# Kernel optimization log

Hardware: AMD Instinct MI355X
Metric: run time of the kernel (lower is better)

The kernel has to match this reference:

```python
import jax, jax.numpy as jnp
import numpy as np

NUM_HEADS = 8


def setup_inputs() -> dict:
    key = jax.random.key(0)
    k1, k2, k3 = jax.random.split(key, 3)
    B, D, H, W = 2, 256, 64, 64
    x = jax.random.normal(k1, (B, D, H, W), dtype=jnp.float32)
    w_qkv = jax.random.normal(k2, (3 * D, D), dtype=jnp.float32) * (D ** -0.5)
    b_qkv = jnp.zeros((3 * D,), dtype=jnp.float32)
    w_proj = jax.random.normal(k3, (D, D), dtype=jnp.float32) * (D ** -0.5)
    b_proj = jnp.zeros((D,), dtype=jnp.float32)
    return {"x": x, "w_qkv": w_qkv, "b_qkv": b_qkv, "w_proj": w_proj, "b_proj": b_proj}


def reference(x, w_qkv, b_qkv, w_proj, b_proj):
    B, D, H, W = x.shape
    N = H * W
    nh = NUM_HEADS
    hd = D // nh
    scale = hd ** -0.5
    # 1x1 conv == per-pixel linear: (B, 3D, H, W)
    qkv = jnp.einsum('od,bdhw->bohw', w_qkv, x) + b_qkv[None, :, None, None]
    # reshape (B, 3, nh, hd, N) then permute to (3, B, nh, N, hd)
    qkv = qkv.reshape(B, 3, nh, hd, N).transpose(1, 0, 2, 4, 3)
    q, k, v = qkv[0], qkv[1], qkv[2]          # each (B, nh, N, hd)
    attn = jnp.einsum('bhnd,bhmd->bhnm', q, k) * scale  # (B, nh, N, N)
    attn = jax.nn.softmax(attn, axis=-1)
    out = jnp.einsum('bhnm,bhmd->bhnd', attn, v)        # (B, nh, N, hd)
    out = out.transpose(0, 1, 3, 2).reshape(B, D, H, W)  # (B, nh, hd, N) -> (B, D, H, W)
    out = jnp.einsum('od,bdhw->bohw', w_proj, out) + b_proj[None, :, None, None]
    return out
```

## Files before the change

kernel.cpp:

```cpp
#include <hip/hip_runtime.h>

typedef unsigned short u16;
typedef unsigned int u32;
typedef float f32x4 __attribute__((ext_vector_type(4)));
typedef float f32x16 __attribute__((ext_vector_type(16)));
typedef __bf16 bf16x8 __attribute__((ext_vector_type(8)));
typedef int i32x4 __attribute__((ext_vector_type(4)));

#define DEV static __device__ __forceinline__

DEV u16 f2bf(float f){
  u32 u = __builtin_bit_cast(u32, f);
  u = (u + 0x7fffu + ((u >> 16) & 1u)) >> 16;
  return (u16)u;
}

DEV float fexp2(float x){
#if __has_builtin(__builtin_amdgcn_exp2f)
  return __builtin_amdgcn_exp2f(x);
#else
  return __builtin_exp2f(x);
#endif
}

DEV void async16(const void* g, void* l){
  __builtin_amdgcn_global_load_lds((const __attribute__((address_space(1))) void*)g,
                                   (__attribute__((address_space(3))) void*)l, 16, 0, 0);
}

static constexpr int NB = 2, DM = 256, NS = 4096, NH = 8, HD = 32;
static constexpr float QSCALE = 0.17677669529663687f * 1.4426950408889634f;
static constexpr float CAP = 24.0f;

__global__ __launch_bounds__(256) void k_transpose_x(const float* __restrict__ x, u16* __restrict__ xT){
  __shared__ float tile[64][65];
  int b = blockIdx.z, dt = blockIdx.y, nt = blockIdx.x;
  int t = threadIdx.x, tr = t >> 4, tc = t & 15;
  const float* src = x + ((size_t)b*DM + dt*64)*NS + nt*64;
#pragma unroll
  for(int rr=0; rr<4; ++rr){
    int row = rr*16 + tr;
    float4 v = *(const float4*)(src + (size_t)row*NS + tc*4);
    tile[row][tc*4+0]=v.x; tile[row][tc*4+1]=v.y; tile[row][tc*4+2]=v.z; tile[row][tc*4+3]=v.w;
  }
  __syncthreads();
#pragma unroll
  for(int rr=0; rr<4; ++rr){
    int nl = rr*16 + tr, dl = tc*4;
    ushort4 o;
    o.x = f2bf(tile[dl+0][nl]); o.y = f2bf(tile[dl+1][nl]);
    o.z = f2bf(tile[dl+2][nl]); o.w = f2bf(tile[dl+3][nl]);
    *(ushort4*)(xT + ((size_t)b*NS + nt*64 + nl)*DM + dt*64 + dl) = o;
  }
}

__global__ __launch_bounds__(256) void k_convert(const float* __restrict__ s, u16* __restrict__ d, int n4){
  int i = blockIdx.x*256 + threadIdx.x;
  if(i < n4){
    float4 v = ((const float4*)s)[i];
    ushort4 o; o.x=f2bf(v.x); o.y=f2bf(v.y); o.z=f2bf(v.z); o.w=f2bf(v.w);
    ((ushort4*)d)[i] = o;
  }
}

template<int MODE>
__global__ __launch_bounds__(256) void k_gemm(const u16* __restrict__ A, const u16* __restrict__ W,
                       const float* __restrict__ bias,
                       u16* __restrict__ q, u16* __restrict__ kbuf, u16* __restrict__ vt,
                       float* __restrict__ outp){
  __shared__ __align__(16) u16 ldsA[32768];
  __shared__ __align__(16) u16 ldsW[32768];
  int b = blockIdx.z, nt = blockIdx.x, ot = blockIdx.y;
  int tid = threadIdx.x;
  const char* Ab = (const char*)(A + ((size_t)b*NS + nt*128)*DM);
  const char* Wb = (const char*)(W + (size_t)ot*128*DM);
#pragma unroll
  for(int it=0; it<16; ++it){
    int dst = it*4096 + tid*16;
    int srcb = dst ^ (((dst >> 9) & 15) << 4);
    async16(Ab + srcb, (char*)ldsA + dst);
    async16(Wb + srcb, (char*)ldsW + dst);
  }
  __syncthreads();
  int w = tid >> 6, l = tid & 63, l15 = l & 15, g = l >> 4;
  f32x4 acc[2][8];
#pragma unroll
  for(int m=0;m<2;++m)
#pragma unroll
    for(int j=0;j<8;++j) acc[m][j] = f32x4{0.f,0.f,0.f,0.f};
#pragma unroll
  for(int kk=0; kk<8; ++kk){
    int cb = kk*64 + g*16;
    bf16x8 a[2], bb[8];
#pragma unroll
    for(int m=0;m<2;++m){
      int row = w*32 + m*16 + l15;
      a[m] = *(const bf16x8*)((const char*)ldsA + row*512 + (cb ^ ((row & 15) << 4)));
    }
#pragma unroll
    for(int j=0;j<8;++j){
      int row = j*16 + l15;
      bb[j] = *(const bf16x8*)((const char*)ldsW + row*512 + (cb ^ ((row & 15) << 4)));
    }
#pragma unroll
    for(int m=0;m<2;++m)
#pragma unroll
      for(int j=0;j<8;++j)
        acc[m][j] = __builtin_amdgcn_mfma_f32_16x16x32_bf16(a[m], bb[j], acc[m][j], 0, 0, 0);
  }

  if constexpr (MODE == 0){
    if(ot < 4){
      float sc = (ot < 2) ? QSCALE : 1.f;
      u16* dst = (ot < 2) ? q : kbuf;
      int hbase = (ot & 1) * 4;
      __syncthreads();
      char* tile = (char*)ldsA;
#pragma unroll
      for(int m=0;m<2;++m){
#pragma unroll
        for(int j=0;j<8;++j){
          int o = j*16 + l15;
          float bs = bias[ot*128 + o];
          float v0 = (acc[m][j][0]+bs)*sc, v1 = (acc[m][j][1]+bs)*sc;
          float v2 = (acc[m][j][2]+bs)*sc, v3 = (acc[m][j][3]+bs)*sc;
          u32 pA, pB;
          asm("v_cvt_pk_bf16_f32 %0, %1, %2" : "=v"(pA) : "v"(v0), "v"(v1));
          asm("v_cvt_pk_bf16_f32 %0, %1, %2" : "=v"(pB) : "v"(v2), "v"(v3));
          int n0 = w*32 + m*16 + g*4;
          *(u16*)(tile + (n0+0)*256 + ((o*2) ^ (((n0+0)&7)<<4))) = (u16)pA;
          *(u16*)(tile + (n0+1)*256 + ((o*2) ^ (((n0+1)&7)<<4))) = (u16)(pA>>16);
          *(u16*)(tile + (n0+2)*256 + ((o*2) ^ (((n0+2)&7)<<4))) = (u16)pB;
          *(u16*)(tile + (n0+3)*256 + ((o*2) ^ (((n0+3)&7)<<4))) = (u16)(pB>>16);
        }
      }
      __syncthreads();
#pragma unroll
      for(int p=0;p<2;++p){
        int seg = p*256 + tid;
        int hsub = seg >> 7, n_l = seg & 127;
        u16* gdst = dst + (((size_t)b*NH + hbase + hsub)*NS + nt*128 + n_l)*HD;
#pragma unroll
        for(int c=0;c<4;++c)
          *(uint4*)((char*)gdst + c*16) =
            *(const uint4*)(tile + n_l*256 + ((hsub*64 + c*16) ^ ((n_l&7)<<4)));
      }
    } else {
#pragma unroll
      for(int m=0;m<2;++m){
        int n0 = nt*128 + w*32 + m*16 + g*4;
#pragma unroll
        for(int j=0;j<8;++j){
          int o = ot*128 + j*16 + l15;
          float bs = bias[o];
          int hh = (o >> 5) & 7, dh = o & 31;
          float v0=acc[m][j][0]+bs, v1=acc[m][j][1]+bs, v2=acc[m][j][2]+bs, v3=acc[m][j][3]+bs;
          u32 pA, pB;
          asm("v_cvt_pk_bf16_f32 %0, %1, %2" : "=v"(pA) : "v"(v0), "v"(v1));
          asm("v_cvt_pk_bf16_f32 %0, %1, %2" : "=v"(pB) : "v"(v2), "v"(v3));
          uint2 pk; pk.x = pA; pk.y = pB;
          *(uint2*)(vt + (((size_t)b*NH + hh)*HD + dh)*NS + n0) = pk;
        }
      }
    }
  } else {
    __syncthreads();
    char* tileF = (char*)ldsA;
#pragma unroll
    for(int m=0;m<2;++m){
#pragma unroll
      for(int j=0;j<8;++j){
        int o = j*16 + l15;
        float bs = bias[ot*128 + o];
        f32x4 v4;
        v4[0]=acc[m][j][0]+bs; v4[1]=acc[m][j][1]+bs;
        v4[2]=acc[m][j][2]+bs; v4[3]=acc[m][j][3]+bs;
        int n0 = w*32 + m*16 + g*4;
        *(f32x4*)(tileF + o*512 + ((n0*4) ^ ((o&7)<<4))) = v4;
      }
    }
    __syncthreads();
#pragma unroll
    for(int p=0;p<4;++p){
      int idx = p*256 + tid;
      int o = idx >> 3, c = idx & 7;
      float* gdst = outp + ((size_t)b*DM + ot*128 + o)*NS + nt*128 + c*16;
#pragma unroll
      for(int u=0;u<4;++u)
        *(uint4*)((char*)gdst + u*16) =
          *(const uint4*)(tileF + o*512 + ((c*64 + u*16) ^ ((o&7)<<4)));
    }
  }
}

__global__ __launch_bounds__(256) void k_attn(const u16* __restrict__ Q, const u16* __restrict__ K,
                       const u16* __restrict__ V, u16* __restrict__ aout){
  __shared__ __align__(16) char lds[32768];
  char* ldsK = lds;
  char* ldsV = lds + 16384;
  int qt = blockIdx.x, bh = blockIdx.y;
  int tid = threadIdx.x, w = tid >> 6, l = tid & 63, l31 = l & 31, hi = l >> 5;
  int kh = w >> 1, qsub = w & 1;
  const u16* Qb = Q + (size_t)bh*NS*HD;
  const u16* Kb = K + (size_t)bh*NS*HD;
  const u16* Vb = V + (size_t)bh*HD*NS;
  int q0w = qt*64 + qsub*32;

  bf16x8 qf[2];
#pragma unroll
  for(int c=0;c<2;++c)
    qf[c] = *(const bf16x8*)(Qb + (size_t)(q0w + l31)*HD + c*16 + hi*8);

  int si = tid >> 7, idx = tid & 127;
  int krow = idx >> 1, khalf = idx & 1;
  int vd = idx >> 2, vch = idx & 3;
  const u16* kg = Kb + (size_t)(si*2048 + krow)*HD + khalf*16;
  const u16* vg = Vb + (size_t)vd*NS + si*2048 + vch*16;
  int kswz0 = (khalf*32 +  0) ^ (((krow >> 1) & 3) << 4);
  int kswz1 = (khalf*32 + 16) ^ (((krow >> 1) & 3) << 4);
  int vswz0 = (vch*32 +  0) ^ ((vd & 7) << 4);
  int vswz1 = (vch*32 + 16) ^ ((vd & 7) << 4);
  char* klw0 = ldsK + si*4096 + krow*64;
  char* vlw0 = ldsV + si*4096 + vd*128;

  {
    uint4 k0 = *(const uint4*)(kg);
    uint4 k1 = *(const uint4*)(kg + 8);
    uint4 v0 = *(const uint4*)(vg);
    uint4 v1 = *(const uint4*)(vg + 8);
    *(uint4*)(klw0 + kswz0) = k0;
    *(uint4*)(klw0 + kswz1) = k1;
    *(uint4*)(vlw0 + vswz0) = v0;
    *(uint4*)(vlw0 + vswz1) = v1;
  }
  __syncthreads();

  f32x16 OT;
#pragma unroll
  for(int r=0;r<16;++r) OT[r] = 0.f;
  f32x16 capv;
#pragma unroll
  for(int r=0;r<16;++r) capv[r] = -CAP;
  float psum = 0.f;

  const char* kfb = ldsK + kh*4096 + l31*64;
  const char* vfb = ldsV + kh*4096 + l31*128;
  int kswA = (hi*16) ^ (((l31 >> 1) & 3) << 4);
  int kswB = (32 + hi*16) ^ (((l31 >> 1) & 3) << 4);

  for(int t=0; t<32; ++t){
    int buf = t & 1;
    uint4 k0, k1, v0, v1;
    if(t < 31){
      const u16* kgt = kg + (size_t)(t+1)*64*HD;
      const u16* vgt = vg + (t+1)*64;
      k0 = *(const uint4*)(kgt); k1 = *(const uint4*)(kgt + 8);
      v0 = *(const uint4*)(vgt); v1 = *(const uint4*)(vgt + 8);
    }
    const char* kf = kfb + buf*8192;
    const char* vf = vfb + buf*8192;
#pragma unroll
    for(int sub=0; sub<2; ++sub){
      bf16x8 ka0 = *(const bf16x8*)(kf + sub*2048 + kswA);
      bf16x8 ka1 = *(const bf16x8*)(kf + sub*2048 + kswB);
      f32x16 st = __builtin_amdgcn_mfma_f32_32x32x16_bf16(ka0, qf[0], capv, 0, 0, 0);
      st = __builtin_amdgcn_mfma_f32_32x32x16_bf16(ka1, qf[1], st, 0, 0, 0);
#pragma unroll
      for(int r=0;r<16;++r) st[r] = fexp2(st[r]);
      {
        float a0 = (st[0]+st[1]) + (st[2]+st[3]);
        float a1 = (st[4]+st[5]) + (st[6]+st[7]);
        float a2 = (st[8]+st[9]) + (st[10]+st[11]);
        float a3 = (st[12]+st[13]) + (st[14]+st[15]);
        psum += (a0+a1) + (a2+a3);
      }
#pragma unroll
      for(int kk=0; kk<2; ++kk){
        int rb = kk*8;
        u32 XA, XB, YA, YB;
        asm("v_cvt_pk_bf16_f32 %0, %1, %2" : "=v"(XA) : "v"(st[rb+0]), "v"(st[rb+1]));
        asm("v_cvt_pk_bf16_f32 %0, %1, %2" : "=v"(XB) : "v"(st[rb+2]), "v"(st[rb+3]));
        asm("v_cvt_pk_bf16_f32 %0, %1, %2" : "=v"(YA) : "v"(st[rb+4]), "v"(st[rb+5]));
        asm("v_cvt_pk_bf16_f32 %0, %1, %2" : "=v"(YB) : "v"(st[rb+6]), "v"(st[rb+7]));
        asm("v_permlane32_swap_b32 %0, %1" : "+v"(XA), "+v"(YA));
        asm("v_permlane32_swap_b32 %0, %1" : "+v"(XB), "+v"(YB));
        i32x4 pw; pw[0] = (int)XA; pw[1] = (int)XB; pw[2] = (int)YA; pw[3] = (int)YB;
        bf16x8 pfrag = __builtin_bit_cast(bf16x8, pw);
        bf16x8 va = *(const bf16x8*)(vf + ((sub*64 + kk*32 + hi*16) ^ ((l31 & 7) << 4)));
        OT = __builtin_amdgcn_mfma_f32_32x32x16_bf16(va, pfrag, OT, 0, 0, 0);
      }
    }
    if(t < 31){
      char* klw = klw0 + (buf^1)*8192;
      char* vlw = vlw0 + (buf^1)*8192;
      *(uint4*)(klw + kswz0) = k0;
      *(uint4*)(klw + kswz1) = k1;
      *(uint4*)(vlw + vswz0) = v0;
      *(uint4*)(vlw + vswz1) = v1;
    }
    __syncthreads();
  }

  float* scrF = (float*)ldsK;
  float* scrS = (float*)ldsV;
  u16* obuf = (u16*)(ldsV + 256);
  float psum2 = psum + __shfl_xor(psum, 32, 64);
  if(kh == 1){
#pragma unroll
    for(int r=0;r<16;++r){
      int dd = (r & 3) + 8*(r >> 2) + 4*hi;
      scrF[qsub*1024 + dd*32 + l31] = OT[r];
    }
    if(hi == 0) scrS[qsub*32 + l31] = psum2;
  }
  __syncthreads();
  if(kh == 0){
    float total = psum2 + scrS[qsub*32 + l31];
    float inv = 1.0f / total;
#pragma unroll
    for(int r=0;r<16;r+=2){
      int dd = (r & 3) + 8*(r >> 2) + 4*hi;
      float o0 = (OT[r]   + scrF[qsub*1024 + dd*32 + l31]) * inv;
      float o1 = (OT[r+1] + scrF[qsub*1024 + (dd+1)*32 + l31]) * inv;
      u32 pk;
      asm("v_cvt_pk_bf16_f32 %0, %1, %2" : "=v"(pk) : "v"(o0), "v"(o1));
      *(u32*)((char*)obuf + (qsub*32 + l31)*64 + dd*2) = pk;
    }
  }
  __syncthreads();
  {
    int b = bh >> 3, h = bh & 7;
    int qq = tid >> 2, ch = tid & 3;
    uint4 vv = *(const uint4*)((const char*)obuf + qq*64 + ch*16);
    *(uint4*)((char*)aout + (((size_t)b*NS + qt*64 + qq)*DM + h*HD)*2 + ch*16) = vv;
  }
}

extern "C" void kernel_launch(void* const* d_in, const int* in_sizes, int n_in,
                              void* d_out, int out_size, void* d_ws, size_t ws_size,
                              hipStream_t stream) {
  (void)in_sizes; (void)n_in; (void)out_size; (void)ws_size;
  const float* x     = (const float*)d_in[0];
  const float* wqkv  = (const float*)d_in[1];
  const float* bqkv  = (const float*)d_in[2];
  const float* wproj = (const float*)d_in[3];
  const float* bproj = (const float*)d_in[4];
  float* out = (float*)d_out;
  char* ws = (char*)d_ws;
  u16* xT  = (u16*)(ws);
  u16* wqb = (u16*)(ws + 4194304);
  u16* wpb = (u16*)(ws + 4587520);
  u16* Q   = (u16*)(ws + 4718592);
  u16* K   = (u16*)(ws + 8912896);
  u16* Vt  = (u16*)(ws + 13107200);
  u16* aout = xT;

  k_transpose_x<<<dim3(64,4,2), 256, 0, stream>>>(x, xT);
  k_convert<<<192, 256, 0, stream>>>(wqkv, wqb, 49152);
  k_convert<<<64, 256, 0, stream>>>(wproj, wpb, 16384);
  k_gemm<0><<<dim3(32,6,2), 256, 0, stream>>>(xT, wqb, bqkv, Q, K, Vt, nullptr);
  k_attn<<<dim3(64,16), 256, 0, stream>>>(Q, K, Vt, aout);
  k_gemm<1><<<dim3(32,2,2), 256, 0, stream>>>(aout, wpb, bproj, nullptr, nullptr, nullptr, out);
}
```

Before: 157.0 us.

## Read K/V directly from global in attention, split keys over 4 waves, fuse prep kernels

The attention kernel no longer stages K and V tiles in LDS with double buffering and barriers. Each wave now loads its MFMA operands straight from global memory, relying on L2 and cache reuse. The block grows to 512 threads, with the key range split four ways, and partial outputs and sums are reduced through LDS. Separately, the x transpose and the two weight conversions are merged into one launch to cut launch overhead. The cost is uncoalesced per-lane global loads and no explicit prefetch overlap, though the barriers go away.

```diff
diff --git a/kernel.cpp b/kernel.cpp
--- a/kernel.cpp
+++ b/kernel.cpp
@@ -32,31 +32,35 @@
 static constexpr float QSCALE = 0.17677669529663687f * 1.4426950408889634f;
 static constexpr float CAP = 24.0f;
 
-__global__ __launch_bounds__(256) void k_transpose_x(const float* __restrict__ x, u16* __restrict__ xT){
+__global__ __launch_bounds__(256) void k_prep(const float* __restrict__ x, u16* __restrict__ xT,
+                      const float* __restrict__ wqkv, u16* __restrict__ wqb,
+                      const float* __restrict__ wproj, u16* __restrict__ wpb){
   __shared__ float tile[64][65];
-  int b = blockIdx.z, dt = blockIdx.y, nt = blockIdx.x;
-  int t = threadIdx.x, tr = t >> 4, tc = t & 15;
-  const float* src = x + ((size_t)b*DM + dt*64)*NS + nt*64;
-#pragma unroll
-  for(int rr=0; rr<4; ++rr){
-    int row = rr*16 + tr;
-    float4 v = *(const float4*)(src + (size_t)row*NS + tc*4);
-    tile[row][tc*4+0]=v.x; tile[row][tc*4+1]=v.y; tile[row][tc*4+2]=v.z; tile[row][tc*4+3]=v.w;
-  }
-  __syncthreads();
-#pragma unroll
-  for(int rr=0; rr<4; ++rr){
-    int nl = rr*16 + tr, dl = tc*4;
-    ushort4 o;
-    o.x = f2bf(tile[dl+0][nl]); o.y = f2bf(tile[dl+1][nl]);
-    o.z = f2bf(tile[dl+2][nl]); o.w = f2bf(tile[dl+3][nl]);
-    *(ushort4*)(xT + ((size_t)b*NS + nt*64 + nl)*DM + dt*64 + dl) = o;
-  }
-}
-
-__global__ __launch_bounds__(256) void k_convert(const float* __restrict__ s, u16* __restrict__ d, int n4){
-  int i = blockIdx.x*256 + threadIdx.x;
-  if(i < n4){
+  int bid = blockIdx.x, t = threadIdx.x;
+  if(bid < 512){
+    int b = bid >> 8, dt = (bid >> 6) & 3, nt = bid & 63;
+    int tr = t >> 4, tc = t & 15;
+    const float* src = x + ((size_t)b*DM + dt*64)*NS + nt*64;
+#pragma unroll
+    for(int rr=0; rr<4; ++rr){
+      int row = rr*16 + tr;
+      float4 v = *(const float4*)(src + (size_t)row*NS + tc*4);
+      tile[row][tc*4+0]=v.x; tile[row][tc*4+1]=v.y; tile[row][tc*4+2]=v.z; tile[row][tc*4+3]=v.w;
+    }
+    __syncthreads();
+#pragma unroll
+    for(int rr=0; rr<4; ++rr){
+      int nl = rr*16 + tr, dl = tc*4;
+      ushort4 o;
+      o.x = f2bf(tile[dl+0][nl]); o.y = f2bf(tile[dl+1][nl]);
+      o.z = f2bf(tile[dl+2][nl]); o.w = f2bf(tile[dl+3][nl]);
+      *(ushort4*)(xT + ((size_t)b*NS + nt*64 + nl)*DM + dt*64 + dl) = o;
+    }
+  } else {
+    int cid = bid - 512;
+    const float* s; u16* d; int i;
+    if(cid < 192){ s = wqkv; d = wqb; i = cid*256 + t; }
+    else         { s = wproj; d = wpb; i = (cid-192)*256 + t; }
     float4 v = ((const float4*)s)[i];
     ushort4 o; o.x=f2bf(v.x); o.y=f2bf(v.y); o.z=f2bf(v.z); o.w=f2bf(v.w);
     ((ushort4*)d)[i] = o;
@@ -193,47 +197,25 @@
   }
 }
 
-__global__ __launch_bounds__(256) void k_attn(const u16* __restrict__ Q, const u16* __restrict__ K,
+__global__ __launch_bounds__(512, 6) void k_attn(const u16* __restrict__ Q, const u16* __restrict__ K,
                        const u16* __restrict__ V, u16* __restrict__ aout){
-  __shared__ __align__(16) char lds[32768];
-  char* ldsK = lds;
-  char* ldsV = lds + 16384;
+  __shared__ float scrO[2][4][32][32];
+  __shared__ float scrS[2][4][32];
+  __shared__ __align__(8) u16 obuf[64][36];
   int qt = blockIdx.x, bh = blockIdx.y;
-  int tid = threadIdx.x, w = tid >> 6, l = tid & 63, l31 = l & 31, hi = l >> 5;
-  int kh = w >> 1, qsub = w & 1;
+  int tid = threadIdx.x, wid = tid >> 6, l = tid & 63, l31 = l & 31, hi = l >> 5;
+  int qsub = wid & 1, kq = wid >> 1;
   const u16* Qb = Q + (size_t)bh*NS*HD;
   const u16* Kb = K + (size_t)bh*NS*HD;
   const u16* Vb = V + (size_t)bh*HD*NS;
-  int q0w = qt*64 + qsub*32;
+  int q0 = qt*64 + qsub*32;
 
   bf16x8 qf[2];
-#pragma unroll
-  for(int c=0;c<2;++c)
-    qf[c] = *(const bf16x8*)(Qb + (size_t)(q0w + l31)*HD + c*16 + hi*8);
-
-  int si = tid >> 7, idx = tid & 127;
-  int krow = idx >> 1, khalf = idx & 1;
-  int vd = idx >> 2, vch = idx & 3;
-  const u16* kg = Kb + (size_t)(si*2048 + krow)*HD + khalf*16;
-  const u16* vg = Vb + (size_t)vd*NS + si*2048 + vch*16;
-  int kswz0 = (khalf*32 +  0) ^ (((krow >> 1) & 3) << 4);
-  int kswz1 = (khalf*32 + 16) ^ (((krow >> 1) & 3) << 4);
-  int vswz0 = (vch*32 +  0) ^ ((vd & 7) << 4);
-  int vswz1 = (vch*32 + 16) ^ ((vd & 7) << 4);
-  char* klw0 = ldsK + si*4096 + krow*64;
-  char* vlw0 = ldsV + si*4096 + vd*128;
-
-  {
-    uint4 k0 = *(const uint4*)(kg);
-    uint4 k1 = *(const uint4*)(kg + 8);
-    uint4 v0 = *(const uint4*)(vg);
-    uint4 v1 = *(const uint4*)(vg + 8);
-    *(uint4*)(klw0 + kswz0) = k0;
-    *(uint4*)(klw0 + kswz1) = k1;
-    *(uint4*)(vlw0 + vswz0) = v0;
-    *(uint4*)(vlw0 + vswz1) = v1;
-  }
-  __syncthreads();
+  qf[0] = *(const bf16x8*)(Qb + (size_t)(q0 + l31)*HD + hi*8);
+  qf[1] = *(const bf16x8*)(Qb + (size_t)(q0 + l31)*HD + 16 + hi*8);
+
+  const u16* kp = Kb + (size_t)(kq*1024 + l31)*HD + hi*8;
+  const u16* vp = Vb + (size_t)l31*NS + kq*1024 + hi*8;
 
   f32x16 OT;
 #pragma unroll
@@ -243,26 +225,12 @@
   for(int r=0;r<16;++r) capv[r] = -CAP;
   float psum = 0.f;
 
-  const char* kfb = ldsK + kh*4096 + l31*64;
-  const char* vfb = ldsV + kh*4096 + l31*128;
-  int kswA = (hi*16) ^ (((l31 >> 1) & 3) << 4);
-  int kswB = (32 + hi*16) ^ (((l31 >> 1) & 3) << 4);
-
-  for(int t=0; t<32; ++t){
-    int buf = t & 1;
-    uint4 k0, k1, v0, v1;
-    if(t < 31){
-      const u16* kgt = kg + (size_t)(t+1)*64*HD;
-      const u16* vgt = vg + (t+1)*64;
-      k0 = *(const uint4*)(kgt); k1 = *(const uint4*)(kgt + 8);
-      v0 = *(const uint4*)(vgt); v1 = *(const uint4*)(vgt + 8);
-    }
-    const char* kf = kfb + buf*8192;
-    const char* vf = vfb + buf*8192;
-#pragma unroll
-    for(int sub=0; sub<2; ++sub){
-      bf16x8 ka0 = *(const bf16x8*)(kf + sub*2048 + kswA);
-      bf16x8 ka1 = *(const bf16x8*)(kf + sub*2048 + kswB);
+  for(int t=0; t<16; ++t){
+#pragma unroll
+    for(int s=0; s<2; ++s){
+      int ks = t*64 + s*32;
+      bf16x8 ka0 = *(const bf16x8*)(kp + (size_t)ks*HD);
+      bf16x8 ka1 = *(const bf16x8*)(kp + (size_t)ks*HD + 16);
       f32x16 st = __builtin_amdgcn_mfma_f32_32x32x16_bf16(ka0, qf[0], capv, 0, 0, 0);
       st = __builtin_amdgcn_mfma_f32_32x32x16_bf16(ka1, qf[1], st, 0, 0, 0);
 #pragma unroll
@@ -286,53 +254,45 @@
         asm("v_permlane32_swap_b32 %0, %1" : "+v"(XB), "+v"(YB));
         i32x4 pw; pw[0] = (int)XA; pw[1] = (int)XB; pw[2] = (int)YA; pw[3] = (int)YB;
         bf16x8 pfrag = __builtin_bit_cast(bf16x8, pw);
-        bf16x8 va = *(const bf16x8*)(vf + ((sub*64 + kk*32 + hi*16) ^ ((l31 & 7) << 4)));
+        bf16x8 va = *(const bf16x8*)(vp + ks + kk*16);
         OT = __builtin_amdgcn_mfma_f32_32x32x16_bf16(va, pfrag, OT, 0, 0, 0);
       }
     }
-    if(t < 31){
-      char* klw = klw0 + (buf^1)*8192;
-      char* vlw = vlw0 + (buf^1)*8192;
-      *(uint4*)(klw + kswz0) = k0;
-      *(uint4*)(klw + kswz1) = k1;
-      *(uint4*)(vlw + vswz0) = v0;
-      *(uint4*)(vlw + vswz1) = v1;
-    }
-    __syncthreads();
-  }
-
-  float* scrF = (float*)ldsK;
-  float* scrS = (float*)ldsV;
-  u16* obuf = (u16*)(ldsV + 256);
+  }
+
   float psum2 = psum + __shfl_xor(psum, 32, 64);
-  if(kh == 1){
-#pragma unroll
-    for(int r=0;r<16;++r){
-      int dd = (r & 3) + 8*(r >> 2) + 4*hi;
-      scrF[qsub*1024 + dd*32 + l31] = OT[r];
-    }
-    if(hi == 0) scrS[qsub*32 + l31] = psum2;
-  }
+#pragma unroll
+  for(int r=0;r<16;++r){
+    int dd = (r & 3) + 8*(r >> 2) + 4*hi;
+    scrO[qsub][kq][dd][l31] = OT[r];
+  }
+  if(hi == 0) scrS[qsub][kq][l31] = psum2;
   __syncthreads();
-  if(kh == 0){
-    float total = psum2 + scrS[qsub*32 + l31];
-    float inv = 1.0f / total;
-#pragma unroll
-    for(int r=0;r<16;r+=2){
-      int dd = (r & 3) + 8*(r >> 2) + 4*hi;
-      float o0 = (OT[r]   + scrF[qsub*1024 + dd*32 + l31]) * inv;
-      float o1 = (OT[r+1] + scrF[qsub*1024 + (dd+1)*32 + l31]) * inv;
-      u32 pk;
-      asm("v_cvt_pk_bf16_f32 %0, %1, %2" : "=v"(pk) : "v"(o0), "v"(o1));
-      *(u32*)((char*)obuf + (qsub*32 + l31)*64 + dd*2) = pk;
-    }
+
+  {
+    int qs = tid >> 8, rem = tid & 255;
+    int qq = rem & 31, d0 = (rem >> 5) * 4;
+    float tot = scrS[qs][0][qq] + scrS[qs][1][qq] + scrS[qs][2][qq] + scrS[qs][3][qq];
+    float inv = 1.0f / tot;
+    float o[4];
+#pragma unroll
+    for(int i=0;i<4;++i){
+      int d = d0 + i;
+      o[i] = (scrO[qs][0][d][qq] + scrO[qs][1][d][qq] + scrO[qs][2][d][qq] + scrO[qs][3][d][qq]) * inv;
+    }
+    u32 pA, pB;
+    asm("v_cvt_pk_bf16_f32 %0, %1, %2" : "=v"(pA) : "v"(o[0]), "v"(o[1]));
+    asm("v_cvt_pk_bf16_f32 %0, %1, %2" : "=v"(pB) : "v"(o[2]), "v"(o[3]));
+    *(u32*)&obuf[qs*32 + qq][d0]     = pA;
+    *(u32*)&obuf[qs*32 + qq][d0 + 2] = pB;
   }
   __syncthreads();
+
   {
     int b = bh >> 3, h = bh & 7;
-    int qq = tid >> 2, ch = tid & 3;
-    uint4 vv = *(const uint4*)((const char*)obuf + qq*64 + ch*16);
-    *(uint4*)((char*)aout + (((size_t)b*NS + qt*64 + qq)*DM + h*HD)*2 + ch*16) = vv;
+    int qq = tid >> 3, ch = tid & 7;
+    uint2 vv = *(const uint2*)((const char*)&obuf[qq][0] + ch*8);
+    *(uint2*)((char*)aout + (((size_t)b*NS + qt*64 + qq)*DM + h*HD)*2 + ch*8) = vv;
   }
 }
 
@@ -355,10 +315,8 @@
   u16* Vt  = (u16*)(ws + 13107200);
   u16* aout = xT;
 
-  k_transpose_x<<<dim3(64,4,2), 256, 0, stream>>>(x, xT);
-  k_convert<<<192, 256, 0, stream>>>(wqkv, wqb, 49152);
-  k_convert<<<64, 256, 0, stream>>>(wproj, wpb, 16384);
+  k_prep<<<768, 256, 0, stream>>>(x, xT, wqkv, wqb, wproj, wpb);
   k_gemm<0><<<dim3(32,6,2), 256, 0, stream>>>(xT, wqb, bqkv, Q, K, Vt, nullptr);
-  k_attn<<<dim3(64,16), 256, 0, stream>>>(Q, K, Vt, aout);
+  k_attn<<<dim3(64,16), 512, 0, stream>>>(Q, K, Vt, aout);
   k_gemm<1><<<dim3(32,2,2), 256, 0, stream>>>(aout, wpb, bproj, nullptr, nullptr, nullptr, out);
 }
```

Measured after the change: 179.8 us. 14.5% more time.

## Use wave-private LDS staging in attention, drop per-tile barriers, merge prep kernels

Applied to the files above, without the earlier changes.

The attention loop now gives each wave its own LDS region for K/V tiles, loaded through registers, so the per-iteration block-wide __syncthreads and the shared double buffer go away. Softmax row sums are now accumulated with an extra MFMA against a ones vector instead of VALU additions and a cross-lane shuffle. The three input-prep kernels are also merged into a single launch to cut launch overhead. The trade-off is that waves sharing a key half now each fetch the same K/V data, doubling L2 reads, and MFMA work rises by half per tile.

```diff
diff --git a/kernel.cpp b/kernel.cpp
--- a/kernel.cpp
+++ b/kernel.cpp
@@ -32,31 +32,35 @@
 static constexpr float QSCALE = 0.17677669529663687f * 1.4426950408889634f;
 static constexpr float CAP = 24.0f;
 
-__global__ __launch_bounds__(256) void k_transpose_x(const float* __restrict__ x, u16* __restrict__ xT){
+__global__ __launch_bounds__(256) void k_prep(const float* __restrict__ x, u16* __restrict__ xT,
+                      const float* __restrict__ wqkv, u16* __restrict__ wqb,
+                      const float* __restrict__ wproj, u16* __restrict__ wpb){
   __shared__ float tile[64][65];
-  int b = blockIdx.z, dt = blockIdx.y, nt = blockIdx.x;
-  int t = threadIdx.x, tr = t >> 4, tc = t & 15;
-  const float* src = x + ((size_t)b*DM + dt*64)*NS + nt*64;
-#pragma unroll
-  for(int rr=0; rr<4; ++rr){
-    int row = rr*16 + tr;
-    float4 v = *(const float4*)(src + (size_t)row*NS + tc*4);
-    tile[row][tc*4+0]=v.x; tile[row][tc*4+1]=v.y; tile[row][tc*4+2]=v.z; tile[row][tc*4+3]=v.w;
-  }
-  __syncthreads();
-#pragma unroll
-  for(int rr=0; rr<4; ++rr){
-    int nl = rr*16 + tr, dl = tc*4;
-    ushort4 o;
-    o.x = f2bf(tile[dl+0][nl]); o.y = f2bf(tile[dl+1][nl]);
-    o.z = f2bf(tile[dl+2][nl]); o.w = f2bf(tile[dl+3][nl]);
-    *(ushort4*)(xT + ((size_t)b*NS + nt*64 + nl)*DM + dt*64 + dl) = o;
-  }
-}
-
-__global__ __launch_bounds__(256) void k_convert(const float* __restrict__ s, u16* __restrict__ d, int n4){
-  int i = blockIdx.x*256 + threadIdx.x;
-  if(i < n4){
+  int bid = blockIdx.x, t = threadIdx.x;
+  if(bid < 512){
+    int b = bid >> 8, dt = (bid >> 6) & 3, nt = bid & 63;
+    int tr = t >> 4, tc = t & 15;
+    const float* src = x + ((size_t)b*DM + dt*64)*NS + nt*64;
+#pragma unroll
+    for(int rr=0; rr<4; ++rr){
+      int row = rr*16 + tr;
+      float4 v = *(const float4*)(src + (size_t)row*NS + tc*4);
+      tile[row][tc*4+0]=v.x; tile[row][tc*4+1]=v.y; tile[row][tc*4+2]=v.z; tile[row][tc*4+3]=v.w;
+    }
+    __syncthreads();
+#pragma unroll
+    for(int rr=0; rr<4; ++rr){
+      int nl = rr*16 + tr, dl = tc*4;
+      ushort4 o;
+      o.x = f2bf(tile[dl+0][nl]); o.y = f2bf(tile[dl+1][nl]);
+      o.z = f2bf(tile[dl+2][nl]); o.w = f2bf(tile[dl+3][nl]);
+      *(ushort4*)(xT + ((size_t)b*NS + nt*64 + nl)*DM + dt*64 + dl) = o;
+    }
+  } else {
+    int cid = bid - 512;
+    const float* s; u16* d; int i;
+    if(cid < 192){ s = wqkv; d = wqb; i = cid*256 + t; }
+    else         { s = wproj; d = wpb; i = (cid-192)*256 + t; }
     float4 v = ((const float4*)s)[i];
     ushort4 o; o.x=f2bf(v.x); o.y=f2bf(v.y); o.z=f2bf(v.z); o.w=f2bf(v.w);
     ((ushort4*)d)[i] = o;
@@ -196,8 +200,6 @@
 __global__ __launch_bounds__(256) void k_attn(const u16* __restrict__ Q, const u16* __restrict__ K,
                        const u16* __restrict__ V, u16* __restrict__ aout){
   __shared__ __align__(16) char lds[32768];
-  char* ldsK = lds;
-  char* ldsV = lds + 16384;
   int qt = blockIdx.x, bh = blockIdx.y;
   int tid = threadIdx.x, w = tid >> 6, l = tid & 63, l31 = l & 31, hi = l >> 5;
   int kh = w >> 1, qsub = w & 1;
@@ -207,73 +209,65 @@
   int q0w = qt*64 + qsub*32;
 
   bf16x8 qf[2];
-#pragma unroll
-  for(int c=0;c<2;++c)
-    qf[c] = *(const bf16x8*)(Qb + (size_t)(q0w + l31)*HD + c*16 + hi*8);
-
-  int si = tid >> 7, idx = tid & 127;
-  int krow = idx >> 1, khalf = idx & 1;
-  int vd = idx >> 2, vch = idx & 3;
-  const u16* kg = Kb + (size_t)(si*2048 + krow)*HD + khalf*16;
-  const u16* vg = Vb + (size_t)vd*NS + si*2048 + vch*16;
-  int kswz0 = (khalf*32 +  0) ^ (((krow >> 1) & 3) << 4);
-  int kswz1 = (khalf*32 + 16) ^ (((krow >> 1) & 3) << 4);
-  int vswz0 = (vch*32 +  0) ^ ((vd & 7) << 4);
-  int vswz1 = (vch*32 + 16) ^ ((vd & 7) << 4);
-  char* klw0 = ldsK + si*4096 + krow*64;
-  char* vlw0 = ldsV + si*4096 + vd*128;
-
+  qf[0] = *(const bf16x8*)(Qb + (size_t)(q0w + l31)*HD + hi*8);
+  qf[1] = *(const bf16x8*)(Qb + (size_t)(q0w + l31)*HD + 16 + hi*8);
+
+  char* myK = lds + w*8192;
+  char* myV = lds + w*8192 + 4096;
+
+  int kwofs[4], vwofs[4];
+#pragma unroll
+  for(int c=0;c<4;++c){
+    int g = c*1024 + l*16;
+    kwofs[c] = g ^ (((g >> 7) & 3) << 4);
+    vwofs[c] = g ^ (((g >> 7) & 7) << 4);
+  }
+  int vrow = (l >> 3), vcol = (l & 7) * 8;
+
+  uint4 kr[4], vr[4];
   {
-    uint4 k0 = *(const uint4*)(kg);
-    uint4 k1 = *(const uint4*)(kg + 8);
-    uint4 v0 = *(const uint4*)(vg);
-    uint4 v1 = *(const uint4*)(vg + 8);
-    *(uint4*)(klw0 + kswz0) = k0;
-    *(uint4*)(klw0 + kswz1) = k1;
-    *(uint4*)(vlw0 + vswz0) = v0;
-    *(uint4*)(vlw0 + vswz1) = v1;
-  }
-  __syncthreads();
-
-  f32x16 OT;
-#pragma unroll
-  for(int r=0;r<16;++r) OT[r] = 0.f;
-  f32x16 capv;
-#pragma unroll
-  for(int r=0;r<16;++r) capv[r] = -CAP;
-  float psum = 0.f;
-
-  const char* kfb = ldsK + kh*4096 + l31*64;
-  const char* vfb = ldsV + kh*4096 + l31*128;
+    const u16* Kg = Kb + (size_t)(kh*2048)*HD;
+    const u16* Vg = Vb + kh*2048;
+#pragma unroll
+    for(int c=0;c<4;++c){
+      kr[c] = *(const uint4*)(Kg + c*512 + l*8);
+      vr[c] = *(const uint4*)(Vg + (size_t)(c*8 + vrow)*NS + vcol);
+    }
+  }
+
+  f32x16 OT, sums, capv;
+#pragma unroll
+  for(int r=0;r<16;++r){ OT[r] = 0.f; sums[r] = 0.f; capv[r] = -CAP; }
+  i32x4 onesw; onesw[0]=0x3F803F80; onesw[1]=0x3F803F80; onesw[2]=0x3F803F80; onesw[3]=0x3F803F80;
+  bf16x8 ones = __builtin_bit_cast(bf16x8, onesw);
+
+  const char* kfb = myK + l31*64;
+  const char* vfb = myV + l31*128;
   int kswA = (hi*16) ^ (((l31 >> 1) & 3) << 4);
   int kswB = (32 + hi*16) ^ (((l31 >> 1) & 3) << 4);
 
   for(int t=0; t<32; ++t){
-    int buf = t & 1;
-    uint4 k0, k1, v0, v1;
+#pragma unroll
+    for(int c=0;c<4;++c) *(uint4*)(myK + kwofs[c]) = kr[c];
+#pragma unroll
+    for(int c=0;c<4;++c) *(uint4*)(myV + vwofs[c]) = vr[c];
     if(t < 31){
-      const u16* kgt = kg + (size_t)(t+1)*64*HD;
-      const u16* vgt = vg + (t+1)*64;
-      k0 = *(const uint4*)(kgt); k1 = *(const uint4*)(kgt + 8);
-      v0 = *(const uint4*)(vgt); v1 = *(const uint4*)(vgt + 8);
-    }
-    const char* kf = kfb + buf*8192;
-    const char* vf = vfb + buf*8192;
+      const u16* Kg = Kb + (size_t)(kh*2048 + (t+1)*64)*HD;
+      const u16* Vg = Vb + kh*2048 + (t+1)*64;
+#pragma unroll
+      for(int c=0;c<4;++c){
+        kr[c] = *(const uint4*)(Kg + c*512 + l*8);
+        vr[c] = *(const uint4*)(Vg + (size_t)(c*8 + vrow)*NS + vcol);
+      }
+    }
 #pragma unroll
     for(int sub=0; sub<2; ++sub){
-      bf16x8 ka0 = *(const bf16x8*)(kf + sub*2048 + kswA);
-      bf16x8 ka1 = *(const bf16x8*)(kf + sub*2048 + kswB);
+      bf16x8 ka0 = *(const bf16x8*)(kfb + sub*2048 + kswA);
+      bf16x8 ka1 = *(const bf16x8*)(kfb + sub*2048 + kswB);
       f32x16 st = __builtin_amdgcn_mfma_f32_32x32x16_bf16(ka0, qf[0], capv, 0, 0, 0);
       st = __builtin_amdgcn_mfma_f32_32x32x16_bf16(ka1, qf[1], st, 0, 0, 0);
 #pragma unroll
       for(int r=0;r<16;++r) st[r] = fexp2(st[r]);
-      {
-        float a0 = (st[0]+st[1]) + (st[2]+st[3]);
-        float a1 = (st[4]+st[5]) + (st[6]+st[7]);
-        float a2 = (st[8]+st[9]) + (st[10]+st[11]);
-        float a3 = (st[12]+st[13]) + (st[14]+st[15]);
-        psum += (a0+a1) + (a2+a3);
-      }
 #pragma unroll
       for(int kk=0; kk<2; ++kk){
         int rb = kk*8;
@@ -286,25 +280,18 @@
         asm("v_permlane32_swap_b32 %0, %1" : "+v"(XB), "+v"(YB));
         i32x4 pw; pw[0] = (int)XA; pw[1] = (int)XB; pw[2] = (int)YA; pw[3] = (int)YB;
         bf16x8 pfrag = __builtin_bit_cast(bf16x8, pw);
-        bf16x8 va = *(const bf16x8*)(vf + ((sub*64 + kk*32 + hi*16) ^ ((l31 & 7) << 4)));
+        sums = __builtin_amdgcn_mfma_f32_32x32x16_bf16(ones, pfrag, sums, 0, 0, 0);
+        bf16x8 va = *(const bf16x8*)(vfb + ((sub*64 + kk*32 + hi*16) ^ ((l31 & 7) << 4)));
         OT = __builtin_amdgcn_mfma_f32_32x32x16_bf16(va, pfrag, OT, 0, 0, 0);
       }
     }
-    if(t < 31){
-      char* klw = klw0 + (buf^1)*8192;
-      char* vlw = vlw0 + (buf^1)*8192;
-      *(uint4*)(klw + kswz0) = k0;
-      *(uint4*)(klw + kswz1) = k1;
-      *(uint4*)(vlw + vswz0) = v0;
-      *(uint4*)(vlw + vswz1) = v1;
-    }
-    __syncthreads();
-  }
-
-  float* scrF = (float*)ldsK;
-  float* scrS = (float*)ldsV;
-  u16* obuf = (u16*)(ldsV + 256);
-  float psum2 = psum + __shfl_xor(psum, 32, 64);
+  }
+
+  float* scrF = (float*)lds;
+  float* scrS = (float*)(lds + 8192);
+  u16* obuf = (u16*)(lds + 8704);
+  float psum2 = sums[0];
+  __syncthreads();
   if(kh == 1){
 #pragma unroll
     for(int r=0;r<16;++r){
@@ -355,9 +342,7 @@
   u16* Vt  = (u16*)(ws + 13107200);
   u16* aout = xT;
 
-  k_transpose_x<<<dim3(64,4,2), 256, 0, stream>>>(x, xT);
-  k_convert<<<192, 256, 0, stream>>>(wqkv, wqb, 49152);
-  k_convert<<<64, 256, 0, stream>>>(wproj, wpb, 16384);
+  k_prep<<<768, 256, 0, stream>>>(x, xT, wqkv, wqb, wproj, wpb);
   k_gemm<0><<<dim3(32,6,2), 256, 0, stream>>>(xT, wqb, bqkv, Q, K, Vt, nullptr);
   k_attn<<<dim3(64,16), 256, 0, stream>>>(Q, K, Vt, aout);
   k_gemm<1><<<dim3(32,2,2), 256, 0, stream>>>(aout, wpb, bproj, nullptr, nullptr, nullptr, out);
```

New measurement: 437.2 us. 178% more time.
